# Kernel tuning notes

Measured on AMD Instinct MI355X. Metric: run time of the kernel, lower is better.

## Reference

```python
import jax, jax.numpy as jnp
import numpy as np

M = 200000   # number of lane candidates
N = 5000     # number of obstacles
NUM_NODE = 150
FEAT = 4


def setup_inputs() -> dict:
    key = jax.random.key(0)
    k1, k2, k3 = jax.random.split(key, 3)
    lane_features = jax.random.normal(k1, (M, NUM_NODE, FEAT), dtype=jnp.float32)
    obs_pos = jax.random.normal(k2, (N, 2), dtype=jnp.float32)
    same_obs_mask = jnp.sort(jax.random.randint(k3, (M, 1), 0, N), axis=0)
    return {"lane_features": lane_features, "obs_pos": obs_pos,
            "same_obs_mask": same_obs_mask}


def reference(lane_features, obs_pos, same_obs_mask):
    lf = lane_features.astype(jnp.float32)          # (M, 150, 4)
    m = lf.shape[0]
    ar = jnp.arange(m)

    # BroadcastObstaclesToLanes: the serial masked-write loop is exactly a gather.
    rep = obs_pos[same_obs_mask[:, 0]].astype(jnp.float32)   # (M, 2)

    # FindClosestNodeFromLineToPoint: interior nodes [1:-1], xy only.
    nodes = lf[:, 1:-1, :2]                          # (M, 148, 2)
    dists = jnp.sum((nodes - rep[:, None, :]) ** 2, axis=-1)  # (M, 148)
    min_idx = jnp.argmin(dists, axis=1) + 1          # (M,), in [1, 148]

    # FindClosestLineSegmentFromLineToPoint (note: distances use all 4 feats,
    # faithfully matching line_nodes[..., :] in the original).
    min_node = lf[ar, min_idx]                       # (M, 4)
    node_prev = lf[ar, min_idx - 1]
    node_next = lf[ar, min_idx + 1]
    dist_prev = jnp.sum((node_prev - min_node) ** 2, axis=1)
    dist_next = jnp.sum((node_next - min_node) ** 2, axis=1)
    min_idx_2nd = jnp.where(dist_next < dist_prev, min_idx + 1, min_idx - 1)
    idx_before = jnp.minimum(min_idx, min_idx_2nd)
    idx_after = jnp.maximum(min_idx, min_idx_2nd)

    # PointToLineProjection on the xy of the chosen segment endpoints.
    seg_s = lf[ar, idx_before, :2]                   # (M, 2)
    seg_e = lf[ar, idx_after, :2]                    # (M, 2)
    line_vec = seg_e - seg_s
    mag = jnp.sqrt(jnp.sum(line_vec ** 2, axis=1, keepdims=True))
    unit = line_vec / mag
    proj_mag = jnp.sum((rep - seg_s) * unit, axis=1, keepdims=True)
    proj_pt = seg_s + proj_mag * unit                # (M, 2)

    indices = jnp.stack([idx_before, idx_after], axis=1)  # (M, 2)
    return proj_pt, indices, rep
```

## Files before the change

kernel.cpp:

```cpp
#include <hip/hip_runtime.h>
#include <math.h>

static constexpr int M_ROWS   = 200000;
static constexpr int NUM_NODE = 150;
static constexpr int ROW_F    = NUM_NODE * 4;
static constexpr int RPW      = 6;
static constexpr int RPB      = 4 * RPW;
static constexpr int GRID     = (M_ROWS + RPB - 1) / RPB;

__global__ __launch_bounds__(256) void obstacle_to_lane_kernel(
    const float* __restrict__ lf,
    const float* __restrict__ obs_pos,
    const int*   __restrict__ mask,
    float*       __restrict__ out)
{
    const int wave = threadIdx.x >> 6;
    const int lane = threadIdx.x & 63;
    const int m0   = blockIdx.x * RPB + wave * RPW;

    int nrows = M_ROWS - m0;
    if (nrows <= 0) return;
    if (nrows > RPW) nrows = RPW;

    const int  j0   = lane;
    const int  j1   = lane + 64;
    const int  j2   = lane + 128;
    const int  j2c  = (j2 < NUM_NODE) ? j2 : (NUM_NODE - 1);
    const bool a0ok = (lane >= 1);
    const bool a2ok = (j2 <= NUM_NODE - 2);

    float2 q0[RPW], q1[RPW], q2[RPW];
    float  rx[RPW], ry[RPW];
    #pragma unroll
    for (int r = 0; r < RPW; ++r) {
        if (r < nrows) {
            const float* row = lf + (size_t)(m0 + r) * ROW_F;
            q0[r] = *reinterpret_cast<const float2*>(row + 4 * j0);
            q1[r] = *reinterpret_cast<const float2*>(row + 4 * j1);
            q2[r] = *reinterpret_cast<const float2*>(row + 4 * j2c);
            const int o = mask[m0 + r];
            rx[r] = obs_pos[2 * o];
            ry[r] = obs_pos[2 * o + 1];
        }
    }

    float bd[RPW];
    int   bj[RPW];
    #pragma unroll
    for (int r = 0; r < RPW; ++r) {
        bd[r] = INFINITY;
        bj[r] = 1 << 30;
        if (r < nrows) {
            float dx, dy, d;
            dx = __fsub_rn(q0[r].x, rx[r]); dy = __fsub_rn(q0[r].y, ry[r]);
            d  = __fadd_rn(__fmul_rn(dx, dx), __fmul_rn(dy, dy));
            if (a0ok && d < bd[r]) { bd[r] = d; bj[r] = j0; }
            dx = __fsub_rn(q1[r].x, rx[r]); dy = __fsub_rn(q1[r].y, ry[r]);
            d  = __fadd_rn(__fmul_rn(dx, dx), __fmul_rn(dy, dy));
            if (d < bd[r]) { bd[r] = d; bj[r] = j1; }
            dx = __fsub_rn(q2[r].x, rx[r]); dy = __fsub_rn(q2[r].y, ry[r]);
            d  = __fadd_rn(__fmul_rn(dx, dx), __fmul_rn(dy, dy));
            if (a2ok && d < bd[r]) { bd[r] = d; bj[r] = j2; }
        }
    }

    #pragma unroll
    for (int off = 32; off > 0; off >>= 1) {
        #pragma unroll
        for (int r = 0; r < RPW; ++r) {
            const float od = __shfl_down(bd[r], off, 64);
            const int   oj = __shfl_down(bj[r], off, 64);
            if (od < bd[r] || (od == bd[r] && oj < bj[r])) { bd[r] = od; bj[r] = oj; }
        }
    }

    #pragma unroll
    for (int r = 0; r < RPW; ++r) {
        if (r < nrows) {
            const int m       = m0 + r;
            const int min_idx = __shfl(bj[r], 0, 64);
            const float* row  = lf + (size_t)m * ROW_F;

            const float4 a = *reinterpret_cast<const float4*>(row + 4 * (min_idx - 1));
            const float4 c = *reinterpret_cast<const float4*>(row + 4 * min_idx);
            const float4 b = *reinterpret_cast<const float4*>(row + 4 * (min_idx + 1));

            float t, s;
            t = __fsub_rn(a.x, c.x); s = __fmul_rn(t, t);
            t = __fsub_rn(a.y, c.y); s = __fadd_rn(s, __fmul_rn(t, t));
            t = __fsub_rn(a.z, c.z); s = __fadd_rn(s, __fmul_rn(t, t));
            t = __fsub_rn(a.w, c.w); s = __fadd_rn(s, __fmul_rn(t, t));
            const float dist_prev = s;
            t = __fsub_rn(b.x, c.x); s = __fmul_rn(t, t);
            t = __fsub_rn(b.y, c.y); s = __fadd_rn(s, __fmul_rn(t, t));
            t = __fsub_rn(b.z, c.z); s = __fadd_rn(s, __fmul_rn(t, t));
            t = __fsub_rn(b.w, c.w); s = __fadd_rn(s, __fmul_rn(t, t));
            const float dist_next = s;

            float sx, sy, ex, ey;
            int ib;
            if (dist_next < dist_prev) {
                ib = min_idx;     sx = c.x; sy = c.y; ex = b.x; ey = b.y;
            } else {
                ib = min_idx - 1; sx = a.x; sy = a.y; ex = c.x; ey = c.y;
            }

            const float lvx = __fsub_rn(ex, sx);
            const float lvy = __fsub_rn(ey, sy);
            const float mag = __fsqrt_rn(__fadd_rn(__fmul_rn(lvx, lvx), __fmul_rn(lvy, lvy)));
            const float ux  = __fdiv_rn(lvx, mag);
            const float uy  = __fdiv_rn(lvy, mag);
            const float pm  = __fadd_rn(__fmul_rn(__fsub_rn(rx[r], sx), ux),
                                        __fmul_rn(__fsub_rn(ry[r], sy), uy));
            const float px  = __fadd_rn(sx, __fmul_rn(pm, ux));
            const float py  = __fadd_rn(sy, __fmul_rn(pm, uy));

            if (lane < 3) {
                float2 v; size_t off;
                if (lane == 0)      { v = make_float2(px, py);                     off = 2 * (size_t)m; }
                else if (lane == 1) { v = make_float2((float)ib, (float)(ib + 1)); off = 2 * (size_t)M_ROWS + 2 * (size_t)m; }
                else                { v = make_float2(rx[r], ry[r]);               off = 4 * (size_t)M_ROWS + 2 * (size_t)m; }
                *reinterpret_cast<float2*>(out + off) = v;
            }
        }
    }
}

extern "C" void kernel_launch(void* const* d_in, const int* in_sizes, int n_in,
                              void* d_out, int out_size, void* d_ws, size_t ws_size,
                              hipStream_t stream) {
    const float* lf      = (const float*)d_in[0];
    const float* obs_pos = (const float*)d_in[1];
    const int*   mask    = (const int*)d_in[2];
    float*       out     = (float*)d_out;

    hipLaunchKernelGGL(obstacle_to_lane_kernel, dim3(GRID), dim3(256), 0, stream,
                       lf, obs_pos, mask, out);
}
```

Before: 626.7 us.

## Persistent waves with double-buffered row batches and shuffle-based neighbor gather

Switches to a persistent grid of 2048 blocks where each wave loops over 4-row batches, prefetching the next batch into registers while computing the current one. Rows are loaded as full float4 nodes so the min node and its neighbors come from cross-lane shuffles instead of a second dependent global load. This targets memory latency exposure and the serialized second load. The cost is twice the register footprint, which may lower occupancy, plus a doubling of per-row load bytes, since the zw components are now fetched for every node.

```diff
diff --git a/kernel.cpp b/kernel.cpp
--- a/kernel.cpp
+++ b/kernel.cpp
@@ -4,9 +4,17 @@
 static constexpr int M_ROWS   = 200000;
 static constexpr int NUM_NODE = 150;
 static constexpr int ROW_F    = NUM_NODE * 4;
-static constexpr int RPW      = 6;
-static constexpr int RPB      = 4 * RPW;
-static constexpr int GRID     = (M_ROWS + RPB - 1) / RPB;
+static constexpr int BPR      = 4;
+static constexpr int NBATCH   = M_ROWS / BPR;
+static constexpr int BLOCKS   = 2048;
+static constexpr int WPB      = 4;
+static constexpr int NWAVES   = BLOCKS * WPB;
+static constexpr int MAX_ITERS = (NBATCH + NWAVES - 1) / NWAVES;
+
+struct Batch {
+    float4 c0[BPR], c1[BPR], c2[BPR];
+    float  rx[BPR], ry[BPR];
+};
 
 __global__ __launch_bounds__(256) void obstacle_to_lane_kernel(
     const float* __restrict__ lf,
@@ -16,93 +24,100 @@
 {
     const int wave = threadIdx.x >> 6;
     const int lane = threadIdx.x & 63;
-    const int m0   = blockIdx.x * RPB + wave * RPW;
-
-    int nrows = M_ROWS - m0;
-    if (nrows <= 0) return;
-    if (nrows > RPW) nrows = RPW;
+    const int wid  = blockIdx.x * WPB + wave;
 
     const int  j0   = lane;
     const int  j1   = lane + 64;
-    const int  j2   = lane + 128;
-    const int  j2c  = (j2 < NUM_NODE) ? j2 : (NUM_NODE - 1);
+    const int  j2c  = (lane + 128 < NUM_NODE) ? (lane + 128) : (NUM_NODE - 1);
     const bool a0ok = (lane >= 1);
-    const bool a2ok = (j2 <= NUM_NODE - 2);
+    const bool a2ok = (lane + 128 <= NUM_NODE - 2);
 
-    float2 q0[RPW], q1[RPW], q2[RPW];
-    float  rx[RPW], ry[RPW];
-    #pragma unroll
-    for (int r = 0; r < RPW; ++r) {
-        if (r < nrows) {
-            const float* row = lf + (size_t)(m0 + r) * ROW_F;
-            q0[r] = *reinterpret_cast<const float2*>(row + 4 * j0);
-            q1[r] = *reinterpret_cast<const float2*>(row + 4 * j1);
-            q2[r] = *reinterpret_cast<const float2*>(row + 4 * j2c);
-            const int o = mask[m0 + r];
-            rx[r] = obs_pos[2 * o];
-            ry[r] = obs_pos[2 * o + 1];
+    Batch A, B;
+
+    auto load = [&](Batch& b, int g) {
+        int o[BPR];
+        #pragma unroll
+        for (int r = 0; r < BPR; ++r) o[r] = mask[g * BPR + r];
+        const float* base = lf + (size_t)g * (BPR * ROW_F);
+        #pragma unroll
+        for (int r = 0; r < BPR; ++r) {
+            const float* row = base + r * ROW_F;
+            b.c0[r] = *reinterpret_cast<const float4*>(row + 4 * j0);
+            b.c1[r] = *reinterpret_cast<const float4*>(row + 4 * j1);
+            b.c2[r] = *reinterpret_cast<const float4*>(row + 4 * j2c);
         }
-    }
+        #pragma unroll
+        for (int r = 0; r < BPR; ++r) {
+            b.rx[r] = obs_pos[2 * o[r]];
+            b.ry[r] = obs_pos[2 * o[r] + 1];
+        }
+    };
 
-    float bd[RPW];
-    int   bj[RPW];
-    #pragma unroll
-    for (int r = 0; r < RPW; ++r) {
-        bd[r] = INFINITY;
-        bj[r] = 1 << 30;
-        if (r < nrows) {
+    auto compute = [&](const Batch& b, int g) {
+        float bd[BPR];
+        int   bj[BPR];
+        #pragma unroll
+        for (int r = 0; r < BPR; ++r) {
+            bd[r] = INFINITY;
+            bj[r] = 1 << 30;
             float dx, dy, d;
-            dx = __fsub_rn(q0[r].x, rx[r]); dy = __fsub_rn(q0[r].y, ry[r]);
+            dx = __fsub_rn(b.c0[r].x, b.rx[r]); dy = __fsub_rn(b.c0[r].y, b.ry[r]);
             d  = __fadd_rn(__fmul_rn(dx, dx), __fmul_rn(dy, dy));
             if (a0ok && d < bd[r]) { bd[r] = d; bj[r] = j0; }
-            dx = __fsub_rn(q1[r].x, rx[r]); dy = __fsub_rn(q1[r].y, ry[r]);
+            dx = __fsub_rn(b.c1[r].x, b.rx[r]); dy = __fsub_rn(b.c1[r].y, b.ry[r]);
             d  = __fadd_rn(__fmul_rn(dx, dx), __fmul_rn(dy, dy));
             if (d < bd[r]) { bd[r] = d; bj[r] = j1; }
-            dx = __fsub_rn(q2[r].x, rx[r]); dy = __fsub_rn(q2[r].y, ry[r]);
+            dx = __fsub_rn(b.c2[r].x, b.rx[r]); dy = __fsub_rn(b.c2[r].y, b.ry[r]);
             d  = __fadd_rn(__fmul_rn(dx, dx), __fmul_rn(dy, dy));
-            if (a2ok && d < bd[r]) { bd[r] = d; bj[r] = j2; }
+            if (a2ok && d < bd[r]) { bd[r] = d; bj[r] = lane + 128; }
         }
-    }
+        #pragma unroll
+        for (int off = 32; off > 0; off >>= 1) {
+            #pragma unroll
+            for (int r = 0; r < BPR; ++r) {
+                const float od = __shfl_down(bd[r], off, 64);
+                const int   oj = __shfl_down(bj[r], off, 64);
+                if (od < bd[r] || (od == bd[r] && oj < bj[r])) { bd[r] = od; bj[r] = oj; }
+            }
+        }
+        #pragma unroll
+        for (int r = 0; r < BPR; ++r) {
+            const int m       = g * BPR + r;
+            const int min_idx = __shfl(bj[r], 0, 64);
 
-    #pragma unroll
-    for (int off = 32; off > 0; off >>= 1) {
-        #pragma unroll
-        for (int r = 0; r < RPW; ++r) {
-            const float od = __shfl_down(bd[r], off, 64);
-            const int   oj = __shfl_down(bj[r], off, 64);
-            if (od < bd[r] || (od == bd[r] && oj < bj[r])) { bd[r] = od; bj[r] = oj; }
-        }
-    }
-
-    #pragma unroll
-    for (int r = 0; r < RPW; ++r) {
-        if (r < nrows) {
-            const int m       = m0 + r;
-            const int min_idx = __shfl(bj[r], 0, 64);
-            const float* row  = lf + (size_t)m * ROW_F;
-
-            const float4 a = *reinterpret_cast<const float4*>(row + 4 * (min_idx - 1));
-            const float4 c = *reinterpret_cast<const float4*>(row + 4 * min_idx);
-            const float4 b = *reinterpret_cast<const float4*>(row + 4 * (min_idx + 1));
+            auto pick = [&](int q) -> float4 {
+                const int sl = q & 63;
+                const int gg = q >> 6;
+                const float4 s = (gg == 0) ? b.c0[r] : ((gg == 1) ? b.c1[r] : b.c2[r]);
+                float4 res;
+                res.x = __shfl(s.x, sl, 64);
+                res.y = __shfl(s.y, sl, 64);
+                res.z = __shfl(s.z, sl, 64);
+                res.w = __shfl(s.w, sl, 64);
+                return res;
+            };
+            const float4 na = pick(min_idx - 1);
+            const float4 nc = pick(min_idx);
+            const float4 nb = pick(min_idx + 1);
 
             float t, s;
-            t = __fsub_rn(a.x, c.x); s = __fmul_rn(t, t);
-            t = __fsub_rn(a.y, c.y); s = __fadd_rn(s, __fmul_rn(t, t));
-            t = __fsub_rn(a.z, c.z); s = __fadd_rn(s, __fmul_rn(t, t));
-            t = __fsub_rn(a.w, c.w); s = __fadd_rn(s, __fmul_rn(t, t));
+            t = __fsub_rn(na.x, nc.x); s = __fmul_rn(t, t);
+            t = __fsub_rn(na.y, nc.y); s = __fadd_rn(s, __fmul_rn(t, t));
+            t = __fsub_rn(na.z, nc.z); s = __fadd_rn(s, __fmul_rn(t, t));
+            t = __fsub_rn(na.w, nc.w); s = __fadd_rn(s, __fmul_rn(t, t));
             const float dist_prev = s;
-            t = __fsub_rn(b.x, c.x); s = __fmul_rn(t, t);
-            t = __fsub_rn(b.y, c.y); s = __fadd_rn(s, __fmul_rn(t, t));
-            t = __fsub_rn(b.z, c.z); s = __fadd_rn(s, __fmul_rn(t, t));
-            t = __fsub_rn(b.w, c.w); s = __fadd_rn(s, __fmul_rn(t, t));
+            t = __fsub_rn(nb.x, nc.x); s = __fmul_rn(t, t);
+            t = __fsub_rn(nb.y, nc.y); s = __fadd_rn(s, __fmul_rn(t, t));
+            t = __fsub_rn(nb.z, nc.z); s = __fadd_rn(s, __fmul_rn(t, t));
+            t = __fsub_rn(nb.w, nc.w); s = __fadd_rn(s, __fmul_rn(t, t));
             const float dist_next = s;
 
             float sx, sy, ex, ey;
             int ib;
             if (dist_next < dist_prev) {
-                ib = min_idx;     sx = c.x; sy = c.y; ex = b.x; ey = b.y;
+                ib = min_idx;     sx = nc.x; sy = nc.y; ex = nb.x; ey = nb.y;
             } else {
-                ib = min_idx - 1; sx = a.x; sy = a.y; ex = c.x; ey = c.y;
+                ib = min_idx - 1; sx = na.x; sy = na.y; ex = nc.x; ey = nc.y;
             }
 
             const float lvx = __fsub_rn(ex, sx);
@@ -110,8 +125,8 @@
             const float mag = __fsqrt_rn(__fadd_rn(__fmul_rn(lvx, lvx), __fmul_rn(lvy, lvy)));
             const float ux  = __fdiv_rn(lvx, mag);
             const float uy  = __fdiv_rn(lvy, mag);
-            const float pm  = __fadd_rn(__fmul_rn(__fsub_rn(rx[r], sx), ux),
-                                        __fmul_rn(__fsub_rn(ry[r], sy), uy));
+            const float pm  = __fadd_rn(__fmul_rn(__fsub_rn(b.rx[r], sx), ux),
+                                        __fmul_rn(__fsub_rn(b.ry[r], sy), uy));
             const float px  = __fadd_rn(sx, __fmul_rn(pm, ux));
             const float py  = __fadd_rn(sy, __fmul_rn(pm, uy));
 
@@ -119,10 +134,25 @@
                 float2 v; size_t off;
                 if (lane == 0)      { v = make_float2(px, py);                     off = 2 * (size_t)m; }
                 else if (lane == 1) { v = make_float2((float)ib, (float)(ib + 1)); off = 2 * (size_t)M_ROWS + 2 * (size_t)m; }
-                else                { v = make_float2(rx[r], ry[r]);               off = 4 * (size_t)M_ROWS + 2 * (size_t)m; }
+                else                { v = make_float2(b.rx[r], b.ry[r]);           off = 4 * (size_t)M_ROWS + 2 * (size_t)m; }
                 *reinterpret_cast<float2*>(out + off) = v;
             }
         }
+    };
+
+    if (wid >= NBATCH) return;
+    load(A, wid);
+    #pragma unroll 1
+    for (int k = 0; k < MAX_ITERS; k += 2) {
+        const int gA = wid + k * NWAVES;
+        const int gB = gA + NWAVES;
+        if (gB < NBATCH) load(B, gB);
+        compute(A, gA);
+        if (gB >= NBATCH) break;
+        const int gA2 = gB + NWAVES;
+        if (gA2 < NBATCH) load(A, gA2);
+        compute(B, gB);
+        if (gA2 >= NBATCH) break;
     }
 }
 
@@ -134,6 +164,6 @@
     const int*   mask    = (const int*)d_in[2];
     float*       out     = (float*)d_out;
 
-    hipLaunchKernelGGL(obstacle_to_lane_kernel, dim3(GRID), dim3(256), 0, stream,
+    hipLaunchKernelGGL(obstacle_to_lane_kernel, dim3(BLOCKS), dim3(256), 0, stream,
                        lf, obs_pos, mask, out);
 }
```

New measurement: 633.5 us. About the same (+1.1%).
